# Kernel tuning notes

Measured on AMD Instinct MI355X. Metric: run time of the kernel, lower is better.

## Reference

```python
import jax, jax.numpy as jnp
import numpy as np

NUM_POS_FEATS = 16
TEMPERATURE = 10000.0
SCALE = 100.0

def sine_pos_embed(x):
    # x: [..., 1] -> [..., NUM_POS_FEATS], interleaved sin/cos per torch get_sine_pos_embed
    i = jnp.arange(NUM_POS_FEATS, dtype=jnp.float32)
    dim_t = TEMPERATURE ** (2.0 * jnp.floor(i / 2.0) / NUM_POS_FEATS)
    emb = x * SCALE / dim_t  # [..., NUM_POS_FEATS]
    s = jnp.sin(emb[..., 0::2])
    c = jnp.cos(emb[..., 1::2])
    return jnp.stack([s, c], axis=-1).reshape(emb.shape)

def setup_inputs() -> dict:
    key = jax.random.key(0)
    ks = jax.random.split(key, 6)
    B, N, D, V, H = 4, 900, 256, 16, 8
    queries = jax.random.normal(ks[0], (B, N, D), jnp.float32)
    current_ref_points = jax.random.uniform(ks[1], (B, N, 4), dtype=jnp.float32)
    prev_ref_points = jax.random.uniform(ks[2], (B, N, 4), dtype=jnp.float32)
    vote_w = jax.random.normal(ks[3], (V * 2, D), jnp.float32) * (1.0 / np.sqrt(D))
    vote_b = jnp.zeros((V * 2,), jnp.float32)
    proj_w = jax.random.normal(ks[4], (H, NUM_POS_FEATS), jnp.float32) * 0.25
    proj_b = jnp.zeros((H,), jnp.float32)
    return {"queries": queries, "current_ref_points": current_ref_points,
            "prev_ref_points": prev_ref_points, "vote_w": vote_w, "vote_b": vote_b,
            "proj_w": proj_w, "proj_b": proj_b}

def reference(queries, current_ref_points, prev_ref_points, vote_w, vote_b, proj_w, proj_b):
    B, N, D = queries.shape
    V = vote_w.shape[0] // 2
    # vote_generator: MLP with num_layers=1 == single Linear
    votes = (queries @ vote_w.T + vote_b).reshape(B, N, V, 2)
    vote_pos = current_ref_points[:, :, None, :2] + votes  # [B,N,V,2]
    centers = current_ref_points[:, :, :2]                  # [B,N,2]
    vf = vote_pos.reshape(B, N * V, 2)
    # squared euclidean distances [B, N*V, N] (cdist then **2)
    d2 = (jnp.sum(vf ** 2, -1)[:, :, None]
          + jnp.sum(centers ** 2, -1)[:, None, :]
          - 2.0 * jnp.einsum('bik,bjk->bij', vf, centers))
    d2 = jnp.maximum(d2, 0.0)
    sigma = jnp.mean(current_ref_points[:, :, 2:], -1, keepdims=True) / 2.0  # [B,N,1]
    sigma_flat = jnp.tile(sigma, (1, V, 1))  # faithful to torch .repeat(1,V,1)
    scores = jnp.exp(-d2 / (2.0 * sigma_flat ** 2))          # [B,N*V,N]
    imap = scores.reshape(B, N, V, N).sum(2)                  # vote-sum -> [B,N,N]
    imap = imap / jnp.maximum(jnp.sum(jnp.abs(imap), 2, keepdims=True), 1e-12)  # F.normalize p=1
    imap = 1.0 - imap
    pos = sine_pos_embed(imap[..., None])                     # [B,N,N,16]
    # pos_proj: 1x1 conv (bias) + ReLU over channel dim
    out = jnp.einsum('bnmf,hf->bhnm', pos, proj_w) + proj_b[None, :, None, None]
    return jax.nn.relu(out)
```

## Files before the change

### kernel.cpp

```cpp
#include <hip/hip_runtime.h>

#define NPF 16
#define NH 8
#define NV 16
#define NN 900
#define ND 256
#define NB 4

__global__ __launch_bounds__(256)
__attribute__((amdgpu_waves_per_eu(4, 4)))
void hough_fused(
    const float* __restrict__ queries,
    const float* __restrict__ cur_ref,
    const float* __restrict__ vote_w,
    const float* __restrict__ vote_b,
    const float* __restrict__ proj_w,
    const float* __restrict__ proj_b,
    float* __restrict__ out)
{
    __shared__ __align__(16) float qs[ND];
    __shared__ float part[256];
    __shared__ float vp[NV * 2];
    __shared__ float s2i[NV];
    __shared__ __align__(16) float4 sCoef[NV];
    __shared__ float red[4];
    __shared__ float s_inv;

    const int tid = threadIdx.x;
    const int bn  = blockIdx.x;
    const int b   = bn / NN;
    const int n   = bn - b * NN;

    qs[tid] = queries[(size_t)bn * ND + tid];
    __syncthreads();

    {
        const int o     = tid & 31;
        const int chunk = tid >> 5;
        const float4* wv = (const float4*)(vote_w + o * ND + chunk * 32);
        const float4* qv = (const float4*)(qs + chunk * 32);
        float p = 0.f;
#pragma unroll
        for (int j = 0; j < 8; j++) {
            float4 w4 = wv[j];
            float4 q4 = qv[j];
            p += w4.x * q4.x + w4.y * q4.y + w4.z * q4.z + w4.w * q4.w;
        }
        part[tid] = p;
    }
    __syncthreads();

    if (tid < 32) {
        float s = vote_b[tid];
#pragma unroll
        for (int c = 0; c < 8; c++) s += part[c * 32 + tid];
        vp[tid] = s + cur_ref[((size_t)b * NN + n) * 4 + (tid & 1)];
    } else if (tid >= 64 && tid < 64 + NV) {
        int v = tid - 64;
        int j = (n * NV + v) % NN;
        float c2 = cur_ref[((size_t)b * NN + j) * 4 + 2];
        float c3 = cur_ref[((size_t)b * NN + j) * 4 + 3];
        float sg = (c2 + c3) * 0.25f;
        s2i[v] = 0.5f / (sg * sg);
    }
    __syncthreads();

    if (tid < NV) {
        float x  = vp[2 * tid];
        float y  = vp[2 * tid + 1];
        float s2 = s2i[tid];
        sCoef[tid] = make_float4(2.f * s2 * x, 2.f * s2 * y,
                                 -s2 * (x * x + y * y), -s2);
    }
    __syncthreads();

    float acc[4] = {0.f, 0.f, 0.f, 0.f};
    const float4* cr4 = (const float4*)cur_ref + (size_t)b * NN;

#pragma unroll 1
    for (int c = 0; c < 2; c++) {
        float ax[8], ay[8], c0[8], ns[8];
#pragma unroll
        for (int v = 0; v < 8; v++) {
            float4 f = sCoef[c * 8 + v];
            ax[v] = f.x; ay[v] = f.y; c0[v] = f.z; ns[v] = f.w;
        }
#pragma unroll
        for (int i = 0; i < 4; i++) {
            int m = tid + 256 * i;
            if (m < NN) {
                float4 cr = cr4[m];
                float cx = cr.x, cy = cr.y;
                float cc = cx * cx + cy * cy;
                float a = 0.f;
#pragma unroll
                for (int v = 0; v < 8; v++) {
                    float t = fmaf(ax[v], cx, c0[v]);
                    t = fmaf(ay[v], cy, t);
                    t = fmaf(ns[v], cc, t);
                    a += __expf(fminf(t, 0.f));
                }
                acc[i] += a;
            }
        }
    }

    float lsum = acc[0] + acc[1] + acc[2] + acc[3];
#pragma unroll
    for (int off = 32; off > 0; off >>= 1) lsum += __shfl_down(lsum, off, 64);
    if ((tid & 63) == 0) red[tid >> 6] = lsum;
    __syncthreads();
    if (tid == 0)
        s_inv = 1.0f / fmaxf(red[0] + red[1] + red[2] + red[3], 1e-12f);
    __syncthreads();
    const float inv = s_inv;

    float xv[4];
#pragma unroll
    for (int i = 0; i < 4; i++) xv[i] = 1.0f - acc[i] * inv;

    const float invt[8] = {100.0f, 31.622776601683793f, 10.0f, 3.1622776601683795f,
                           1.0f, 0.31622776601683794f, 0.1f, 0.031622776601683791f};

    float* outbase = out + (((size_t)(b * NH) * NN + n) * NN);

#pragma unroll 1
    for (int pass = 0; pass < 2; pass++) {
        float Wr[64];
#pragma unroll
        for (int k = 0; k < 64; k++) Wr[k] = proj_w[pass * 64 + k];
        float Pb[4];
#pragma unroll
        for (int h = 0; h < 4; h++) Pb[h] = proj_b[pass * 4 + h];

        float* opass = outbase + (size_t)pass * 4 * NN * NN;

#pragma unroll
        for (int i = 0; i < 4; i++) {
            int m = tid + 256 * i;
            if (m < NN) {
                float x = xv[i];
                float sk[8], ck[8];
#pragma unroll
                for (int k = 0; k < 8; k++) {
                    float a = x * invt[k];
                    sk[k] = __sinf(a);
                    ck[k] = __cosf(a);
                }
                float* op = opass + m;
#pragma unroll
                for (int h = 0; h < 4; h++) {
                    float o = Pb[h];
#pragma unroll
                    for (int k = 0; k < 8; k++) {
                        o = fmaf(Wr[h * 16 + 2 * k],     sk[k], o);
                        o = fmaf(Wr[h * 16 + 2 * k + 1], ck[k], o);
                    }
                    op[(size_t)h * NN * NN] = fmaxf(o, 0.f);
                }
            }
        }
    }
}

extern "C" void kernel_launch(void* const* d_in, const int* in_sizes, int n_in,
                              void* d_out, int out_size, void* d_ws, size_t ws_size,
                              hipStream_t stream) {
    const float* queries = (const float*)d_in[0];
    const float* cur_ref = (const float*)d_in[1];
    const float* vote_w  = (const float*)d_in[3];
    const float* vote_b  = (const float*)d_in[4];
    const float* proj_w  = (const float*)d_in[5];
    const float* proj_b  = (const float*)d_in[6];
    float* out = (float*)d_out;

    hough_fused<<<NB * NN, 256, 0, stream>>>(queries, cur_ref, vote_w, vote_b,
                                             proj_w, proj_b, out);
}
```

Baseline: 151.2 us.

## Split fused kernel into imap and flat epilogue kernels via workspace

Splits the single fused kernel into two launches. The first computes the normalized influence map and writes it to a workspace buffer. The second is a flat elementwise kernel that reads each value, computes the sine/cos embedding and writes all eight heads, with the projection weights held in shared memory. The aim is to remove the register pressure and poor occupancy of the fused epilogue, at the cost of an extra launch and a round trip of about 13MB through global memory.

```diff
diff --git a/kernel.cpp b/kernel.cpp
--- a/kernel.cpp
+++ b/kernel.cpp
@@ -6,17 +6,15 @@
 #define NN 900
 #define ND 256
 #define NB 4
+#define NM (NN * NN)
+#define TOTAL (NB * NM)
 
-__global__ __launch_bounds__(256)
-__attribute__((amdgpu_waves_per_eu(4, 4)))
-void hough_fused(
+__global__ __launch_bounds__(256) void hough_imap(
     const float* __restrict__ queries,
     const float* __restrict__ cur_ref,
     const float* __restrict__ vote_w,
     const float* __restrict__ vote_b,
-    const float* __restrict__ proj_w,
-    const float* __restrict__ proj_b,
-    float* __restrict__ out)
+    float* __restrict__ xbuf)
 {
     __shared__ __align__(16) float qs[ND];
     __shared__ float part[256];
@@ -115,51 +113,63 @@
     __syncthreads();
     const float inv = s_inv;
 
-    float xv[4];
+    float* xr = xbuf + (size_t)bn * NN;
 #pragma unroll
-    for (int i = 0; i < 4; i++) xv[i] = 1.0f - acc[i] * inv;
+    for (int i = 0; i < 4; i++) {
+        int m = tid + 256 * i;
+        if (m < NN) xr[m] = 1.0f - acc[i] * inv;
+    }
+}
+
+__global__ __launch_bounds__(256) void hough_epi(
+    const float* __restrict__ xbuf,
+    const float* __restrict__ proj_w,
+    const float* __restrict__ proj_b,
+    float* __restrict__ out)
+{
+    __shared__ __align__(16) float4 sW[NH * 4];
+    __shared__ float sB[NH];
+
+    const int tid = threadIdx.x;
+    if (tid < NH * 4) sW[tid] = ((const float4*)proj_w)[tid];
+    if (tid < NH) sB[tid] = proj_b[tid];
+    __syncthreads();
+
+    const int id = blockIdx.x * 256 + tid;
+    if (id >= TOTAL) return;
+
+    const float x = xbuf[id];
 
     const float invt[8] = {100.0f, 31.622776601683793f, 10.0f, 3.1622776601683795f,
                            1.0f, 0.31622776601683794f, 0.1f, 0.031622776601683791f};
+    float sk[8], ck[8];
+#pragma unroll
+    for (int k = 0; k < 8; k++) {
+        float a = x * invt[k];
+        sk[k] = __sinf(a);
+        ck[k] = __cosf(a);
+    }
 
-    float* outbase = out + (((size_t)(b * NH) * NN + n) * NN);
-
-#pragma unroll 1
-    for (int pass = 0; pass < 2; pass++) {
-        float Wr[64];
-#pragma unroll
-        for (int k = 0; k < 64; k++) Wr[k] = proj_w[pass * 64 + k];
-        float Pb[4];
-#pragma unroll
-        for (int h = 0; h < 4; h++) Pb[h] = proj_b[pass * 4 + h];
-
-        float* opass = outbase + (size_t)pass * 4 * NN * NN;
+    const int b = id / NM;
+    const int r = id - b * NM;
+    float* op = out + (size_t)b * NH * NM + r;
 
 #pragma unroll
-        for (int i = 0; i < 4; i++) {
-            int m = tid + 256 * i;
-            if (m < NN) {
-                float x = xv[i];
-                float sk[8], ck[8];
-#pragma unroll
-                for (int k = 0; k < 8; k++) {
-                    float a = x * invt[k];
-                    sk[k] = __sinf(a);
-                    ck[k] = __cosf(a);
-                }
-                float* op = opass + m;
-#pragma unroll
-                for (int h = 0; h < 4; h++) {
-                    float o = Pb[h];
-#pragma unroll
-                    for (int k = 0; k < 8; k++) {
-                        o = fmaf(Wr[h * 16 + 2 * k],     sk[k], o);
-                        o = fmaf(Wr[h * 16 + 2 * k + 1], ck[k], o);
-                    }
-                    op[(size_t)h * NN * NN] = fmaxf(o, 0.f);
-                }
-            }
-        }
+    for (int h = 0; h < NH; h++) {
+        const float4 w0 = sW[h * 4 + 0];
+        const float4 w1 = sW[h * 4 + 1];
+        const float4 w2 = sW[h * 4 + 2];
+        const float4 w3 = sW[h * 4 + 3];
+        float o = sB[h];
+        o = fmaf(w0.x, sk[0], o); o = fmaf(w0.y, ck[0], o);
+        o = fmaf(w0.z, sk[1], o); o = fmaf(w0.w, ck[1], o);
+        o = fmaf(w1.x, sk[2], o); o = fmaf(w1.y, ck[2], o);
+        o = fmaf(w1.z, sk[3], o); o = fmaf(w1.w, ck[3], o);
+        o = fmaf(w2.x, sk[4], o); o = fmaf(w2.y, ck[4], o);
+        o = fmaf(w2.z, sk[5], o); o = fmaf(w2.w, ck[5], o);
+        o = fmaf(w3.x, sk[6], o); o = fmaf(w3.y, ck[6], o);
+        o = fmaf(w3.z, sk[7], o); o = fmaf(w3.w, ck[7], o);
+        op[(size_t)h * NM] = fmaxf(o, 0.f);
     }
 }
 
@@ -172,8 +182,9 @@
     const float* vote_b  = (const float*)d_in[4];
     const float* proj_w  = (const float*)d_in[5];
     const float* proj_b  = (const float*)d_in[6];
-    float* out = (float*)d_out;
+    float* out  = (float*)d_out;
+    float* xbuf = (float*)d_ws;
 
-    hough_fused<<<NB * NN, 256, 0, stream>>>(queries, cur_ref, vote_w, vote_b,
-                                             proj_w, proj_b, out);
+    hough_imap<<<NB * NN, 256, 0, stream>>>(queries, cur_ref, vote_w, vote_b, xbuf);
+    hough_epi<<<(TOTAL + 255) / 256, 256, 0, stream>>>(xbuf, proj_w, proj_b, out);
 }
```

After: 153.6 us. No clear change (+1.6%).

## Split fused kernel into imap kernel and flat elementwise epilogue kernel

Applied to the files above, without the earlier changes.

Breaks the single fused kernel in two. The first kernel computes the normalized interaction map, writes 1-imap to a workspace buffer, and drops the heavy projection registers. The second is a flat grid that reads x, computes the sin/cos features once, and writes 8 heads in 4 passes, loading weights as wave-uniform scalars. The aim is to raise occupancy and let both phases use dense flat indexing, at the cost of an extra global round trip for the B*N*N map and a second kernel launch.

```diff
diff --git a/kernel.cpp b/kernel.cpp
--- a/kernel.cpp
+++ b/kernel.cpp
@@ -6,17 +6,16 @@
 #define NN 900
 #define ND 256
 #define NB 4
-
-__global__ __launch_bounds__(256)
-__attribute__((amdgpu_waves_per_eu(4, 4)))
-void hough_fused(
+#define NM (NN * NN)
+#define TOTAL (NB * NM)
+#define EPB 1024
+
+__global__ __launch_bounds__(256) void hough_imap(
     const float* __restrict__ queries,
     const float* __restrict__ cur_ref,
     const float* __restrict__ vote_w,
     const float* __restrict__ vote_b,
-    const float* __restrict__ proj_w,
-    const float* __restrict__ proj_b,
-    float* __restrict__ out)
+    float* __restrict__ xbuf)
 {
     __shared__ __align__(16) float qs[ND];
     __shared__ float part[256];
@@ -115,49 +114,72 @@
     __syncthreads();
     const float inv = s_inv;
 
-    float xv[4];
-#pragma unroll
-    for (int i = 0; i < 4; i++) xv[i] = 1.0f - acc[i] * inv;
+    float* xr = xbuf + (size_t)bn * NN;
+#pragma unroll
+    for (int i = 0; i < 4; i++) {
+        int m = tid + 256 * i;
+        if (m < NN) xr[m] = 1.0f - acc[i] * inv;
+    }
+}
+
+__device__ __forceinline__ float uload(const float* p) {
+    return __int_as_float(__builtin_amdgcn_readfirstlane(__float_as_int(*p)));
+}
+
+__global__ __launch_bounds__(256)
+__attribute__((amdgpu_waves_per_eu(4, 4)))
+void hough_epi(
+    const float* __restrict__ xbuf,
+    const float* __restrict__ proj_w,
+    const float* __restrict__ proj_b,
+    float* __restrict__ out)
+{
+    const int tid  = threadIdx.x;
+    const int base = blockIdx.x * EPB + tid;
 
     const float invt[8] = {100.0f, 31.622776601683793f, 10.0f, 3.1622776601683795f,
                            1.0f, 0.31622776601683794f, 0.1f, 0.031622776601683791f};
 
-    float* outbase = out + (((size_t)(b * NH) * NN + n) * NN);
+    float sk[4][8], ck[4][8];
+    float* op[4];
+    bool ok[4];
+#pragma unroll
+    for (int i = 0; i < 4; i++) {
+        int id = base + 256 * i;
+        ok[i] = (id < TOTAL);
+        float x = ok[i] ? xbuf[id] : 0.f;
+#pragma unroll
+        for (int k = 0; k < 8; k++) {
+            float a = x * invt[k];
+            sk[i][k] = __sinf(a);
+            ck[i][k] = __cosf(a);
+        }
+        unsigned int b = (unsigned int)id / (unsigned int)NM;
+        unsigned int r = (unsigned int)id - b * (unsigned int)NM;
+        op[i] = out + (size_t)b * NH * NM + r;
+    }
 
 #pragma unroll 1
-    for (int pass = 0; pass < 2; pass++) {
-        float Wr[64];
-#pragma unroll
-        for (int k = 0; k < 64; k++) Wr[k] = proj_w[pass * 64 + k];
-        float Pb[4];
-#pragma unroll
-        for (int h = 0; h < 4; h++) Pb[h] = proj_b[pass * 4 + h];
-
-        float* opass = outbase + (size_t)pass * 4 * NN * NN;
+    for (int pass = 0; pass < 4; pass++) {
+        float w[32];
+#pragma unroll
+        for (int k = 0; k < 32; k++) w[k] = uload(proj_w + pass * 32 + k);
+        const float b0 = uload(proj_b + pass * 2 + 0);
+        const float b1 = uload(proj_b + pass * 2 + 1);
 
 #pragma unroll
         for (int i = 0; i < 4; i++) {
-            int m = tid + 256 * i;
-            if (m < NN) {
-                float x = xv[i];
-                float sk[8], ck[8];
-#pragma unroll
-                for (int k = 0; k < 8; k++) {
-                    float a = x * invt[k];
-                    sk[k] = __sinf(a);
-                    ck[k] = __cosf(a);
-                }
-                float* op = opass + m;
-#pragma unroll
-                for (int h = 0; h < 4; h++) {
-                    float o = Pb[h];
-#pragma unroll
-                    for (int k = 0; k < 8; k++) {
-                        o = fmaf(Wr[h * 16 + 2 * k],     sk[k], o);
-                        o = fmaf(Wr[h * 16 + 2 * k + 1], ck[k], o);
-                    }
-                    op[(size_t)h * NN * NN] = fmaxf(o, 0.f);
-                }
+            float o0 = b0, o1 = b1;
+#pragma unroll
+            for (int k = 0; k < 8; k++) {
+                o0 = fmaf(w[2 * k],          sk[i][k], o0);
+                o0 = fmaf(w[2 * k + 1],      ck[i][k], o0);
+                o1 = fmaf(w[16 + 2 * k],     sk[i][k], o1);
+                o1 = fmaf(w[16 + 2 * k + 1], ck[i][k], o1);
+            }
+            if (ok[i]) {
+                op[i][(size_t)(pass * 2 + 0) * NM] = fmaxf(o0, 0.f);
+                op[i][(size_t)(pass * 2 + 1) * NM] = fmaxf(o1, 0.f);
             }
         }
     }
@@ -172,8 +194,9 @@
     const float* vote_b  = (const float*)d_in[4];
     const float* proj_w  = (const float*)d_in[5];
     const float* proj_b  = (const float*)d_in[6];
-    float* out = (float*)d_out;
-
-    hough_fused<<<NB * NN, 256, 0, stream>>>(queries, cur_ref, vote_w, vote_b,
-                                             proj_w, proj_b, out);
-}
+    float* out  = (float*)d_out;
+    float* xbuf = (float*)d_ws;
+
+    hough_imap<<<NB * NN, 256, 0, stream>>>(queries, cur_ref, vote_w, vote_b, xbuf);
+    hough_epi<<<(TOTAL + EPB - 1) / EPB, 256, 0, stream>>>(xbuf, proj_w, proj_b, out);
+}
```

Measured after the change: 153.6 us. Within noise of the previous version (+1.6%).

## Pack sin/cos and proj weights into fp16 pairs and use fdot2 projection

Applied to the files above, without the earlier changes.

Computes sin/cos once per column and packs each pair into fp16 half2. The 16-feature projection then runs as 8 packed fdot2 ops per head, replacing 16 fp32 FMAs, and the two 4-head passes that recomputed sin/cos are merged into one. Weights are loaded once via readfirstlane so they can live in scalar registers, and the waves_per_eu upper bound is relaxed to allow more occupancy. This trades fp32 precision for fp16 (round-toward-zero) in the projection inputs, which adds numerical error.

```diff
diff --git a/kernel.cpp b/kernel.cpp
--- a/kernel.cpp
+++ b/kernel.cpp
@@ -6,9 +6,27 @@
 #define NN 900
 #define ND 256
 #define NB 4
+#define NM (NN * NN)
+
+typedef __fp16 half2v __attribute__((ext_vector_type(2)));
+union h2u { half2v h; unsigned int u; float f; };
+
+#if __has_builtin(__builtin_amdgcn_fdot2)
+__device__ __forceinline__ float fdot2f(half2v a, half2v b, float c) {
+    return __builtin_amdgcn_fdot2(a, b, c, false);
+}
+#else
+__device__ __forceinline__ float fdot2f(half2v a, half2v b, float c) {
+    return fmaf((float)a.x, (float)b.x, fmaf((float)a.y, (float)b.y, c));
+}
+#endif
+
+__device__ __forceinline__ float uloadf(const float* p) {
+    return __int_as_float(__builtin_amdgcn_readfirstlane(__float_as_int(*p)));
+}
 
 __global__ __launch_bounds__(256)
-__attribute__((amdgpu_waves_per_eu(4, 4)))
+__attribute__((amdgpu_waves_per_eu(4, 8)))
 void hough_fused(
     const float* __restrict__ queries,
     const float* __restrict__ cur_ref,
@@ -115,49 +133,45 @@
     __syncthreads();
     const float inv = s_inv;
 
-    float xv[4];
-#pragma unroll
-    for (int i = 0; i < 4; i++) xv[i] = 1.0f - acc[i] * inv;
-
     const float invt[8] = {100.0f, 31.622776601683793f, 10.0f, 3.1622776601683795f,
                            1.0f, 0.31622776601683794f, 0.1f, 0.031622776601683791f};
+    half2v skck[4][8];
+#pragma unroll
+    for (int i = 0; i < 4; i++) {
+        float x = 1.0f - acc[i] * inv;
+#pragma unroll
+        for (int k = 0; k < 8; k++) {
+            float a = x * invt[k];
+            skck[i][k] = __builtin_amdgcn_cvt_pkrtz(__sinf(a), __cosf(a));
+        }
+    }
 
-    float* outbase = out + (((size_t)(b * NH) * NN + n) * NN);
+    half2v W[64];
+#pragma unroll
+    for (int j = 0; j < 64; j++) {
+        h2u u;
+        u.h = __builtin_amdgcn_cvt_pkrtz(uloadf(proj_w + 2 * j),
+                                         uloadf(proj_w + 2 * j + 1));
+        u.u = __builtin_amdgcn_readfirstlane(u.u);
+        W[j] = u.h;
+    }
+    float Pb[NH];
+#pragma unroll
+    for (int h = 0; h < NH; h++) Pb[h] = uloadf(proj_b + h);
 
-#pragma unroll 1
-    for (int pass = 0; pass < 2; pass++) {
-        float Wr[64];
+    float* outrow = out + ((size_t)(b * NH) * NN + n) * NN;
 #pragma unroll
-        for (int k = 0; k < 64; k++) Wr[k] = proj_w[pass * 64 + k];
-        float Pb[4];
+    for (int i = 0; i < 4; i++) {
+        int m = tid + 256 * i;
+        if (m < NN) {
+            float* op = outrow + m;
 #pragma unroll
-        for (int h = 0; h < 4; h++) Pb[h] = proj_b[pass * 4 + h];
-
-        float* opass = outbase + (size_t)pass * 4 * NN * NN;
-
+            for (int h = 0; h < NH; h++) {
+                float o = Pb[h];
 #pragma unroll
-        for (int i = 0; i < 4; i++) {
-            int m = tid + 256 * i;
-            if (m < NN) {
-                float x = xv[i];
-                float sk[8], ck[8];
-#pragma unroll
-                for (int k = 0; k < 8; k++) {
-                    float a = x * invt[k];
-                    sk[k] = __sinf(a);
-                    ck[k] = __cosf(a);
-                }
-                float* op = opass + m;
-#pragma unroll
-                for (int h = 0; h < 4; h++) {
-                    float o = Pb[h];
-#pragma unroll
-                    for (int k = 0; k < 8; k++) {
-                        o = fmaf(Wr[h * 16 + 2 * k],     sk[k], o);
-                        o = fmaf(Wr[h * 16 + 2 * k + 1], ck[k], o);
-                    }
-                    op[(size_t)h * NN * NN] = fmaxf(o, 0.f);
-                }
+                for (int k = 0; k < 8; k++)
+                    o = fdot2f(skck[i][k], W[h * 8 + k], o);
+                op[(size_t)h * NM] = fmaxf(o, 0.f);
             }
         }
     }
```

Result: no change. 149.1 us (-1.4%).
